# Kernel optimization log

Hardware: AMD Instinct MI355X
Metric: run time of the kernel (lower is better)

Reference implementation:

```python
import jax, jax.numpy as jnp
import numpy as np

N = 10000      # nodes
E = 160000     # edges
G = 512        # graphs in batch
IN, H, OUT = 128, 512, 16
L = 4          # num_layers
EPS = 1e-5


def setup_inputs() -> dict:
    key = jax.random.key(0)
    ks = jax.random.split(key, 8)
    x = jax.random.normal(ks[0], (N, IN), dtype=jnp.float32)
    edge_index = jax.random.randint(ks[1], (2, E), 0, N)
    batch = jnp.sort(jax.random.randint(ks[2], (N,), 0, G))
    # GCNConv layer 0 (IN -> H) and layers 1..L-1 (H -> H), plus per-layer LayerNorm affine
    W0 = jax.random.normal(ks[3], (IN, H), dtype=jnp.float32) / np.float32(np.sqrt(IN))
    b0 = jnp.zeros((H,), jnp.float32)
    g0 = jnp.ones((IN,), jnp.float32)
    be0 = jnp.zeros((IN,), jnp.float32)
    Wh = jax.random.normal(ks[4], (L - 1, H, H), dtype=jnp.float32) / np.float32(np.sqrt(H))
    bh = jnp.zeros((L - 1, H), jnp.float32)
    gh = jnp.ones((L - 1, H), jnp.float32)
    beh = jnp.zeros((L - 1, H), jnp.float32)
    linW = jax.random.normal(ks[5], (H, OUT), dtype=jnp.float32) / np.float32(np.sqrt(H))
    linb = jnp.zeros((OUT,), jnp.float32)
    return dict(x=x, edge_index=edge_index, batch=batch, W0=W0, b0=b0, g0=g0, be0=be0,
                Wh=Wh, bh=bh, gh=gh, beh=beh, linW=linW, linb=linb)


def _layernorm(x, g, b):
    mu = jnp.mean(x, axis=-1, keepdims=True)
    var = jnp.var(x, axis=-1, keepdims=True)
    return (x - mu) * jax.lax.rsqrt(var + EPS) * g + b


def _gcn(x, W, b, src, dst, dinv):
    # GCNConv with self-loops: out_i = sum_{j->i} d_j^-1/2 d_i^-1/2 (xW)_j + d_i^-1 (xW)_i + b
    h = x @ W                                   # [N, H']
    coef = (dinv[src] * dinv[dst])[:, None]     # [E, 1]
    agg = jax.ops.segment_sum(h[src] * coef, dst, num_segments=N)
    agg = agg + h * (dinv * dinv)[:, None]      # self-loop term
    return agg + b


def reference(x, edge_index, batch, W0, b0, g0, be0, Wh, bh, gh, beh, linW, linb):
    src, dst = edge_index[0], edge_index[1]
    # degree with self-loops (counted on destination nodes, edge weight 1)
    deg = jax.ops.segment_sum(jnp.ones((E,), x.dtype), dst, num_segments=N) + 1.0
    dinv = jax.lax.rsqrt(deg)
    h = jax.nn.relu(_gcn(_layernorm(x, g0, be0), W0, b0, src, dst, dinv))
    for i in range(L - 1):
        h = jax.nn.relu(_gcn(_layernorm(h, gh[i], beh[i]), Wh[i], bh[i], src, dst, dinv))
    # scatter-mean pooling by graph id
    counts = jax.ops.segment_sum(jnp.ones((N,), x.dtype), batch, num_segments=G)
    pooled = jax.ops.segment_sum(h, batch, num_segments=G) / jnp.maximum(counts, 1.0)[:, None]
    return pooled @ linW + linb
```

## Files before the change

kernel.cpp:

```cpp
#include <hip/hip_runtime.h>

#define NN 10000
#define NE 160000
#define NG 512
#define DIN 128
#define DH 512
#define DOUT 16
#define NPAD 10112

typedef __bf16 bf16_t;
typedef __attribute__((ext_vector_type(8))) __bf16 bf16x8;
typedef __attribute__((ext_vector_type(2))) __bf16 bf16x2;
typedef __attribute__((ext_vector_type(4))) float f32x4;


__global__ void k_deg_count(const int* __restrict__ dst, int* __restrict__ deg) {
    int e = blockIdx.x * blockDim.x + threadIdx.x;
    if (e < NE) atomicAdd(&deg[dst[e]], 1);
}

__global__ void k_dinv(const int* __restrict__ deg, float* __restrict__ dinv) {
    int n = blockIdx.x * blockDim.x + threadIdx.x;
    if (n < NN) dinv[n] = rsqrtf((float)deg[n] + 1.0f);
}

__global__ __launch_bounds__(1024) void k_scan(const int* __restrict__ cnt, int* __restrict__ rowptr) {
    __shared__ int part[1024];
    int tid = threadIdx.x;
    const int PER = 10;
    int base = tid * PER;
    int local[PER];
    int s = 0;
#pragma unroll
    for (int i = 0; i < PER; ++i) {
        int idx = base + i;
        int v = (idx < NN) ? cnt[idx] : 0;
        local[i] = s;
        s += v;
    }
    part[tid] = s;
    __syncthreads();
    for (int off = 1; off < 1024; off <<= 1) {
        int v = (tid >= off) ? part[tid - off] : 0;
        __syncthreads();
        part[tid] += v;
        __syncthreads();
    }
    int offset = (tid > 0) ? part[tid - 1] : 0;
#pragma unroll
    for (int i = 0; i < PER; ++i) {
        int idx = base + i;
        if (idx < NN) rowptr[idx] = offset + local[i];
    }
    if (tid == 1023) rowptr[NN] = part[1023];
}

__global__ void k_fill_csr(const int* __restrict__ src, const int* __restrict__ dst,
                           const float* __restrict__ dinv, const int* __restrict__ rowptr,
                           int* __restrict__ cursor, int* __restrict__ csr_src,
                           float* __restrict__ csr_coef) {
    int e = blockIdx.x * blockDim.x + threadIdx.x;
    if (e >= NE) return;
    int s = src[e], d = dst[e];
    int pos = atomicAdd(&cursor[d], 1);
    int idx = rowptr[d] + pos;
    csr_src[idx] = s;
    csr_coef[idx] = dinv[s] * dinv[d];
}


__global__ void k_wt_all(const float* __restrict__ W0, const float* __restrict__ Wh,
                         bf16_t* __restrict__ Wt0, bf16_t* __restrict__ Wth) {
    int idx = blockIdx.x * 256 + threadIdx.x;
    if (idx < 512 * DIN) {
        int k = idx >> 9, n = idx & 511;
        Wt0[n * DIN + k] = (bf16_t)W0[idx];
    }
    int j = idx - 512 * DIN;
    if (j >= 0 && j < 3 * DH * DH) {
        int l = j / (DH * DH), r = j % (DH * DH);
        int k = r >> 9, n = r & 511;
        Wth[(size_t)l * DH * DH + n * DH + k] = (bf16_t)Wh[j];
    }
}


__global__ __launch_bounds__(256) void k_ln0(const float* __restrict__ x,
                                             const float* __restrict__ g,
                                             const float* __restrict__ b,
                                             bf16_t* __restrict__ y) {
    int row = blockIdx.x * 4 + (threadIdx.x >> 6);
    int lane = threadIdx.x & 63;
    if (row >= NN) return;
    const float* xr = x + (size_t)row * DIN;
    float v0 = xr[lane], v1 = xr[lane + 64];
    float s = v0 + v1, s2 = v0 * v0 + v1 * v1;
#pragma unroll
    for (int off = 32; off; off >>= 1) {
        s += __shfl_xor(s, off);
        s2 += __shfl_xor(s2, off);
    }
    float mu = s * (1.f / 128.f);
    float var = s2 * (1.f / 128.f) - mu * mu;
    float r = rsqrtf(var + 1e-5f);
    bf16_t* yr = y + (size_t)row * DIN;
    yr[lane] = (bf16_t)((v0 - mu) * r * g[lane] + b[lane]);
    yr[lane + 64] = (bf16_t)((v1 - mu) * r * g[lane + 64] + b[lane + 64]);
}


__global__ __launch_bounds__(256) void k_ln512(const bf16_t* __restrict__ x,
                                               const float* __restrict__ g,
                                               const float* __restrict__ b,
                                               bf16_t* __restrict__ y) {
    int row = blockIdx.x * 4 + (threadIdx.x >> 6);
    int lane = threadIdx.x & 63;
    if (row >= NN) return;
    int c0 = lane * 8;
    bf16x8 v = *(const bf16x8*)&x[(size_t)row * DH + c0];
    float f[8];
    float s = 0.f, s2 = 0.f;
#pragma unroll
    for (int i = 0; i < 8; ++i) {
        f[i] = (float)v[i];
        s += f[i];
        s2 += f[i] * f[i];
    }
#pragma unroll
    for (int off = 32; off; off >>= 1) {
        s += __shfl_xor(s, off);
        s2 += __shfl_xor(s2, off);
    }
    float mu = s * (1.f / 512.f);
    float var = s2 * (1.f / 512.f) - mu * mu;
    float r = rsqrtf(var + 1e-5f);
    f32x4 g0 = *(const f32x4*)&g[c0], g1 = *(const f32x4*)&g[c0 + 4];
    f32x4 b0 = *(const f32x4*)&b[c0], b1 = *(const f32x4*)&b[c0 + 4];
    bf16x8 o;
#pragma unroll
    for (int i = 0; i < 4; ++i) {
        o[i] = (bf16_t)((f[i] - mu) * r * g0[i] + b0[i]);
        o[i + 4] = (bf16_t)((f[i + 4] - mu) * r * g1[i] + b1[i]);
    }
    *(bf16x8*)&y[(size_t)row * DH + c0] = o;
}


template <bool EPI>
__global__ __launch_bounds__(256) void k_gemm_bf16(const bf16_t* __restrict__ A,
                                                   const bf16_t* __restrict__ Bt,
                                                   const float* __restrict__ bias,
                                                   bf16_t* __restrict__ C, int K) {
    __shared__ bf16_t As[128 * 64];
    __shared__ bf16_t Bs[64 * 64];
    int tid = threadIdx.x;
    int lane = tid & 63, w = tid >> 6;
    int row0 = blockIdx.x * 128;
    int col0 = blockIdx.y * 64;
    int wm = w >> 1, wn = w & 1;

    f32x4 acc[4][2];
#pragma unroll
    for (int i = 0; i < 4; ++i)
#pragma unroll
        for (int j = 0; j < 2; ++j) acc[i][j] = (f32x4){0.f, 0.f, 0.f, 0.f};

    int lr = lane >> 3;
    int lc = lane & 7;

    for (int kt = 0; kt < K; kt += 64) {
#pragma unroll
        for (int i = 0; i < 4; ++i) {
            int r = w * 32 + i * 8 + lr;
            int cg = lc ^ (r & 7);
            const bf16_t* src = A + (size_t)(row0 + r) * K + kt + cg * 8;
            __builtin_amdgcn_global_load_lds(
                (const __attribute__((address_space(1))) void*)src,
                (__attribute__((address_space(3))) void*)(As + (w * 32 + i * 8) * 64),
                16, 0, 0);
        }
#pragma unroll
        for (int i = 0; i < 2; ++i) {
            int r = w * 16 + i * 8 + lr;
            int cg = lc ^ (r & 7);
            const bf16_t* src = Bt + (size_t)(col0 + r) * K + kt + cg * 8;
            __builtin_amdgcn_global_load_lds(
                (const __attribute__((address_space(1))) void*)src,
                (__attribute__((address_space(3))) void*)(Bs + (w * 16 + i * 8) * 64),
                16, 0, 0);
        }
        __syncthreads();
#pragma unroll
        for (int ks = 0; ks < 2; ++ks) {
            bf16x8 af[4], bfr[2];
#pragma unroll
            for (int mi = 0; mi < 4; ++mi) {
                int mr = wm * 64 + mi * 16 + (lane & 15);
                int c = (ks * 4 + (lane >> 4)) ^ (mr & 7);
                af[mi] = *(const bf16x8*)&As[mr * 64 + c * 8];
            }
#pragma unroll
            for (int ni = 0; ni < 2; ++ni) {
                int nr = wn * 32 + ni * 16 + (lane & 15);
                int c = (ks * 4 + (lane >> 4)) ^ (nr & 7);
                bfr[ni] = *(const bf16x8*)&Bs[nr * 64 + c * 8];
            }
#pragma unroll
            for (int mi = 0; mi < 4; ++mi)
#pragma unroll
                for (int ni = 0; ni < 2; ++ni)
                    acc[mi][ni] = __builtin_amdgcn_mfma_f32_16x16x32_bf16(
                        af[mi], bfr[ni], acc[mi][ni], 0, 0, 0);
        }
        __syncthreads();
    }
#pragma unroll
    for (int mi = 0; mi < 4; ++mi)
#pragma unroll
        for (int ni = 0; ni < 2; ++ni) {
            int col = col0 + wn * 32 + ni * 16 + (lane & 15);
            float bv = EPI ? bias[col] : 0.f;
#pragma unroll
            for (int q = 0; q < 4; ++q) {
                int row = row0 + wm * 64 + mi * 16 + (lane >> 4) * 4 + q;
                float v = acc[mi][ni][q];
                if (EPI) v = fmaxf(v + bv, 0.f);
                C[(size_t)row * DH + col] = (bf16_t)v;
            }
        }
}


__global__ __launch_bounds__(256) void k_agg128(const bf16_t* __restrict__ H,
                                                const int* __restrict__ rowptr,
                                                const int* __restrict__ csr_src,
                                                const float* __restrict__ csr_coef,
                                                const float* __restrict__ dinv,
                                                bf16_t* __restrict__ out) {
    int w = threadIdx.x >> 6, lane = threadIdx.x & 63;
    int n = blockIdx.x * 4 + w;
    int c0 = lane * 2;
    float a0 = 0.f, a1 = 0.f;
    int s0 = rowptr[n], s1 = rowptr[n + 1];
    int k = s0;
    for (; k + 2 <= s1; k += 2) {
        int sA = csr_src[k], sB = csr_src[k + 1];
        float cA = csr_coef[k], cB = csr_coef[k + 1];
        bf16x2 vA = *(const bf16x2*)&H[(size_t)sA * DIN + c0];
        bf16x2 vB = *(const bf16x2*)&H[(size_t)sB * DIN + c0];
        a0 += (float)vA[0] * cA + (float)vB[0] * cB;
        a1 += (float)vA[1] * cA + (float)vB[1] * cB;
    }
    if (k < s1) {
        int sA = csr_src[k];
        float cA = csr_coef[k];
        bf16x2 vA = *(const bf16x2*)&H[(size_t)sA * DIN + c0];
        a0 += (float)vA[0] * cA;
        a1 += (float)vA[1] * cA;
    }
    float di = dinv[n], sc = di * di;
    bf16x2 vs = *(const bf16x2*)&H[(size_t)n * DIN + c0];
    a0 += (float)vs[0] * sc;
    a1 += (float)vs[1] * sc;
    bf16x2 o;
    o[0] = (bf16_t)a0;
    o[1] = (bf16_t)a1;
    *(bf16x2*)&out[(size_t)n * DIN + c0] = o;
}


template <bool DO_LN>
__global__ __launch_bounds__(256) void k_agg(const bf16_t* __restrict__ H,
                                             const int* __restrict__ rowptr,
                                             const int* __restrict__ csr_src,
                                             const float* __restrict__ csr_coef,
                                             const float* __restrict__ dinv,
                                             const float* __restrict__ bias,
                                             const float* __restrict__ gamma,
                                             const float* __restrict__ beta,
                                             bf16_t* __restrict__ out) {
    int w = threadIdx.x >> 6, lane = threadIdx.x & 63;
    int n = blockIdx.x * 4 + w;
    int c0 = lane * 8;
    float acc[8] = {0.f, 0.f, 0.f, 0.f, 0.f, 0.f, 0.f, 0.f};
    int s0 = rowptr[n], s1 = rowptr[n + 1];
    int k = s0;
    for (; k + 2 <= s1; k += 2) {
        int sA = csr_src[k], sB = csr_src[k + 1];
        float cA = csr_coef[k], cB = csr_coef[k + 1];
        bf16x8 vA = *(const bf16x8*)&H[(size_t)sA * DH + c0];
        bf16x8 vB = *(const bf16x8*)&H[(size_t)sB * DH + c0];
#pragma unroll
        for (int i = 0; i < 8; ++i) acc[i] += (float)vA[i] * cA + (float)vB[i] * cB;
    }
    if (k < s1) {
        int sA = csr_src[k];
        float cA = csr_coef[k];
        bf16x8 vA = *(const bf16x8*)&H[(size_t)sA * DH + c0];
#pragma unroll
        for (int i = 0; i < 8; ++i) acc[i] += (float)vA[i] * cA;
    }
    float di = dinv[n], sc = di * di;
    bf16x8 vs = *(const bf16x8*)&H[(size_t)n * DH + c0];
#pragma unroll
    for (int i = 0; i < 8; ++i) acc[i] += (float)vs[i] * sc;
    f32x4 bb0 = *(const f32x4*)&bias[c0], bb1 = *(const f32x4*)&bias[c0 + 4];
#pragma unroll
    for (int i = 0; i < 4; ++i) {
        acc[i] = fmaxf(acc[i] + bb0[i], 0.f);
        acc[i + 4] = fmaxf(acc[i + 4] + bb1[i], 0.f);
    }
    bf16x8 o;
    if (DO_LN) {
        float s = 0.f, s2 = 0.f;
#pragma unroll
        for (int i = 0; i < 8; ++i) {
            s += acc[i];
            s2 += acc[i] * acc[i];
        }
#pragma unroll
        for (int off = 32; off; off >>= 1) {
            s += __shfl_xor(s, off);
            s2 += __shfl_xor(s2, off);
        }
        float mu = s * (1.f / 512.f);
        float var = s2 * (1.f / 512.f) - mu * mu;
        float r = rsqrtf(var + 1e-5f);
        f32x4 g0 = *(const f32x4*)&gamma[c0], g1 = *(const f32x4*)&gamma[c0 + 4];
        f32x4 be0 = *(const f32x4*)&beta[c0], be1 = *(const f32x4*)&beta[c0 + 4];
#pragma unroll
        for (int i = 0; i < 4; ++i) {
            o[i] = (bf16_t)((acc[i] - mu) * r * g0[i] + be0[i]);
            o[i + 4] = (bf16_t)((acc[i + 4] - mu) * r * g1[i] + be1[i]);
        }
    } else {
#pragma unroll
        for (int i = 0; i < 8; ++i) o[i] = (bf16_t)acc[i];
    }
    *(bf16x8*)&out[(size_t)n * DH + c0] = o;
}


__global__ __launch_bounds__(256) void k_poolfin(const bf16_t* __restrict__ h,
                                                 const int* __restrict__ batch,
                                                 const float* __restrict__ linW,
                                                 const float* __restrict__ linb,
                                                 float* __restrict__ out) {
    __shared__ float pooled[DH];
    __shared__ float red[256];
    int g = blockIdx.x;
    int t = threadIdx.x;
    int lo = 0, hi = NN;
    while (lo < hi) {
        int mid = (lo + hi) >> 1;
        if (batch[mid] < g) lo = mid + 1;
        else hi = mid;
    }
    int start = lo;
    hi = NN;
    while (lo < hi) {
        int mid = (lo + hi) >> 1;
        if (batch[mid] < g + 1) lo = mid + 1;
        else hi = mid;
    }
    int end = lo;
    int c0 = t * 2;
    float a0 = 0.f, a1 = 0.f;
    for (int i = start; i < end; ++i) {
        bf16x2 v = *(const bf16x2*)&h[(size_t)i * DH + c0];
        a0 += (float)v[0];
        a1 += (float)v[1];
    }
    float inv = 1.f / fmaxf((float)(end - start), 1.0f);
    pooled[c0] = a0 * inv;
    pooled[c0 + 1] = a1 * inv;
    __syncthreads();
    int o = t & 15, c = t >> 4;
    float s = 0.f;
    int k0 = c * 32;
    for (int k = k0; k < k0 + 32; ++k) s += pooled[k] * linW[k * DOUT + o];
    red[t] = s;
    __syncthreads();
    if (t < DOUT) {
        float acc2 = 0.f;
        for (int cc = 0; cc < 16; ++cc) acc2 += red[cc * 16 + t];
        out[g * DOUT + t] = acc2 + linb[t];
    }
}


extern "C" void kernel_launch(void* const* d_in, const int* in_sizes, int n_in,
                              void* d_out, int out_size, void* d_ws, size_t ws_size,
                              hipStream_t stream) {
    const float* x = (const float*)d_in[0];
    const int* ei = (const int*)d_in[1];
    const int* batch = (const int*)d_in[2];
    const float* W0 = (const float*)d_in[3];
    const float* b0 = (const float*)d_in[4];
    const float* g0 = (const float*)d_in[5];
    const float* be0 = (const float*)d_in[6];
    const float* Wh = (const float*)d_in[7];
    const float* bh = (const float*)d_in[8];
    const float* gh = (const float*)d_in[9];
    const float* beh = (const float*)d_in[10];
    const float* linW = (const float*)d_in[11];
    const float* linb = (const float*)d_in[12];
    float* out = (float*)d_out;

    bf16_t* lnbuf = (bf16_t*)d_ws;
    bf16_t* Cbf = lnbuf + (size_t)NPAD * DH;
    bf16_t* lnx = Cbf + (size_t)NPAD * DH;
    bf16_t* aggx = lnx + (size_t)NPAD * DIN;
    bf16_t* Wt0 = aggx + (size_t)NPAD * DIN;
    bf16_t* Wth = Wt0 + 512 * DIN;
    float* dinv = (float*)(Wth + 3 * 512 * 512);
    int* deg = (int*)(dinv + NN);
    int* rowptr = deg + NN;
    int* cursor = rowptr + NN + 1;
    int* csr_src = cursor + NN;
    float* csr_coef = (float*)(csr_src + NE);

    const int* srcp = ei;
    const int* dstp = ei + NE;

    hipMemsetAsync(deg, 0, NN * sizeof(int), stream);
    hipMemsetAsync(cursor, 0, NN * sizeof(int), stream);
    k_deg_count<<<(NE + 255) / 256, 256, 0, stream>>>(dstp, deg);
    k_dinv<<<(NN + 255) / 256, 256, 0, stream>>>(deg, dinv);
    k_scan<<<1, 1024, 0, stream>>>(deg, rowptr);
    k_fill_csr<<<(NE + 255) / 256, 256, 0, stream>>>(srcp, dstp, dinv, rowptr, cursor,
                                                     csr_src, csr_coef);
    k_wt_all<<<(512 * DIN + 3 * DH * DH + 255) / 256, 256, 0, stream>>>(W0, Wh, Wt0, Wth);

    dim3 gemm_grid(NPAD / 128, DH / 64);

    k_ln0<<<(NN + 3) / 4, 256, 0, stream>>>(x, g0, be0, lnx);
    k_agg128<<<NN / 4, 256, 0, stream>>>(lnx, rowptr, csr_src, csr_coef, dinv, aggx);
    k_gemm_bf16<true><<<gemm_grid, 256, 0, stream>>>(aggx, Wt0, b0, Cbf, DIN);
    k_ln512<<<(NN + 3) / 4, 256, 0, stream>>>(Cbf, gh + 0 * DH, beh + 0 * DH, lnbuf);

    for (int l = 0; l < 2; ++l) {
        k_gemm_bf16<false><<<gemm_grid, 256, 0, stream>>>(lnbuf, Wth + (size_t)l * DH * DH,
                                                          nullptr, Cbf, DH);
        k_agg<true><<<NN / 4, 256, 0, stream>>>(Cbf, rowptr, csr_src, csr_coef, dinv,
                                                bh + l * DH, gh + (l + 1) * DH,
                                                beh + (l + 1) * DH, lnbuf);
    }
    k_gemm_bf16<false><<<gemm_grid, 256, 0, stream>>>(lnbuf, Wth + (size_t)2 * DH * DH,
                                                      nullptr, Cbf, DH);
    k_agg<false><<<NN / 4, 256, 0, stream>>>(Cbf, rowptr, csr_src, csr_coef, dinv,
                                             bh + 2 * DH, nullptr, nullptr, lnbuf);

    k_poolfin<<<NG, 256, 0, stream>>>(lnbuf, batch, linW, linb, out);
}
```

Before: 235.4 us.

## Fuse prep kernels, interleave CSR, shrink GEMM tile, split aggregation across warps

Merges the input LayerNorm, degree count, weight transpose and cursor reset into one multi-role prep kernel, and folds the dinv computation into the scan. The CSR source index and coefficient are packed into one int2 array so each edge needs a single load. GEMM tiles shrink from 128x64 to 64x64 so more blocks are launched. Aggregation now gives each node a whole block, with four warps splitting its edges and summing partials in shared memory. This trades fewer launches and more parallelism for an extra block-level reduction and sync in every aggregation.

```diff
diff --git a/kernel.cpp b/kernel.cpp
--- a/kernel.cpp
+++ b/kernel.cpp
@@ -12,19 +12,70 @@
 typedef __attribute__((ext_vector_type(8))) __bf16 bf16x8;
 typedef __attribute__((ext_vector_type(2))) __bf16 bf16x2;
 typedef __attribute__((ext_vector_type(4))) float f32x4;
-
-
-__global__ void k_deg_count(const int* __restrict__ dst, int* __restrict__ deg) {
-    int e = blockIdx.x * blockDim.x + threadIdx.x;
-    if (e < NE) atomicAdd(&deg[dst[e]], 1);
-}
-
-__global__ void k_dinv(const int* __restrict__ deg, float* __restrict__ dinv) {
-    int n = blockIdx.x * blockDim.x + threadIdx.x;
-    if (n < NN) dinv[n] = rsqrtf((float)deg[n] + 1.0f);
-}
-
-__global__ __launch_bounds__(1024) void k_scan(const int* __restrict__ cnt, int* __restrict__ rowptr) {
+typedef __attribute__((ext_vector_type(2))) float f32x2;
+
+#define LNB 2500
+#define DEGB ((NE + 255) / 256)
+#define WTE (512 * DIN + 3 * DH * DH)
+#define WTB ((WTE + 255) / 256)
+#define CURB ((NN + 255) / 256)
+
+
+__global__ __launch_bounds__(256) void k_prep(const float* __restrict__ x,
+                                              const float* __restrict__ g0,
+                                              const float* __restrict__ be0,
+                                              bf16_t* __restrict__ lnx,
+                                              const int* __restrict__ dst,
+                                              int* __restrict__ deg,
+                                              const float* __restrict__ W0,
+                                              const float* __restrict__ Wh,
+                                              bf16_t* __restrict__ Wt0,
+                                              bf16_t* __restrict__ Wth,
+                                              int* __restrict__ cursor) {
+    int b = blockIdx.x;
+    int tid = threadIdx.x;
+    if (b < LNB) {
+        int row = b * 4 + (tid >> 6);
+        int lane = tid & 63;
+        const float* xr = x + (size_t)row * DIN;
+        float v0 = xr[lane], v1 = xr[lane + 64];
+        float s = v0 + v1, s2 = v0 * v0 + v1 * v1;
+#pragma unroll
+        for (int off = 32; off; off >>= 1) {
+            s += __shfl_xor(s, off);
+            s2 += __shfl_xor(s2, off);
+        }
+        float mu = s * (1.f / 128.f);
+        float var = s2 * (1.f / 128.f) - mu * mu;
+        float r = rsqrtf(var + 1e-5f);
+        bf16_t* yr = lnx + (size_t)row * DIN;
+        yr[lane] = (bf16_t)((v0 - mu) * r * g0[lane] + be0[lane]);
+        yr[lane + 64] = (bf16_t)((v1 - mu) * r * g0[lane + 64] + be0[lane + 64]);
+    } else if (b < LNB + DEGB) {
+        int e = (b - LNB) * 256 + tid;
+        if (e < NE) atomicAdd(&deg[dst[e]], 1);
+    } else if (b < LNB + DEGB + WTB) {
+        int idx = (b - LNB - DEGB) * 256 + tid;
+        if (idx < 512 * DIN) {
+            int k = idx >> 9, n = idx & 511;
+            Wt0[n * DIN + k] = (bf16_t)W0[idx];
+        } else if (idx < WTE) {
+            int j = idx - 512 * DIN;
+            int l = j >> 18;
+            int r2 = j & 262143;
+            int k = r2 >> 9, n = r2 & 511;
+            Wth[((size_t)l << 18) + n * DH + k] = (bf16_t)Wh[j];
+        }
+    } else {
+        int i = (b - LNB - DEGB - WTB) * 256 + tid;
+        if (i < NN) cursor[i] = 0;
+    }
+}
+
+
+__global__ __launch_bounds__(1024) void k_scan(const int* __restrict__ cnt,
+                                               int* __restrict__ rowptr,
+                                               float* __restrict__ dinv) {
     __shared__ int part[1024];
     int tid = threadIdx.x;
     const int PER = 10;
@@ -35,6 +86,7 @@
     for (int i = 0; i < PER; ++i) {
         int idx = base + i;
         int v = (idx < NN) ? cnt[idx] : 0;
+        if (idx < NN) dinv[idx] = rsqrtf((float)v + 1.0f);
         local[i] = s;
         s += v;
     }
@@ -57,55 +109,12 @@
 
 __global__ void k_fill_csr(const int* __restrict__ src, const int* __restrict__ dst,
                            const float* __restrict__ dinv, const int* __restrict__ rowptr,
-                           int* __restrict__ cursor, int* __restrict__ csr_src,
-                           float* __restrict__ csr_coef) {
+                           int* __restrict__ cursor, int2* __restrict__ csr) {
     int e = blockIdx.x * blockDim.x + threadIdx.x;
     if (e >= NE) return;
     int s = src[e], d = dst[e];
     int pos = atomicAdd(&cursor[d], 1);
-    int idx = rowptr[d] + pos;
-    csr_src[idx] = s;
-    csr_coef[idx] = dinv[s] * dinv[d];
-}
-
-
-__global__ void k_wt_all(const float* __restrict__ W0, const float* __restrict__ Wh,
-                         bf16_t* __restrict__ Wt0, bf16_t* __restrict__ Wth) {
-    int idx = blockIdx.x * 256 + threadIdx.x;
-    if (idx < 512 * DIN) {
-        int k = idx >> 9, n = idx & 511;
-        Wt0[n * DIN + k] = (bf16_t)W0[idx];
-    }
-    int j = idx - 512 * DIN;
-    if (j >= 0 && j < 3 * DH * DH) {
-        int l = j / (DH * DH), r = j % (DH * DH);
-        int k = r >> 9, n = r & 511;
-        Wth[(size_t)l * DH * DH + n * DH + k] = (bf16_t)Wh[j];
-    }
-}
-
-
-__global__ __launch_bounds__(256) void k_ln0(const float* __restrict__ x,
-                                             const float* __restrict__ g,
-                                             const float* __restrict__ b,
-                                             bf16_t* __restrict__ y) {
-    int row = blockIdx.x * 4 + (threadIdx.x >> 6);
-    int lane = threadIdx.x & 63;
-    if (row >= NN) return;
-    const float* xr = x + (size_t)row * DIN;
-    float v0 = xr[lane], v1 = xr[lane + 64];
-    float s = v0 + v1, s2 = v0 * v0 + v1 * v1;
-#pragma unroll
-    for (int off = 32; off; off >>= 1) {
-        s += __shfl_xor(s, off);
-        s2 += __shfl_xor(s2, off);
-    }
-    float mu = s * (1.f / 128.f);
-    float var = s2 * (1.f / 128.f) - mu * mu;
-    float r = rsqrtf(var + 1e-5f);
-    bf16_t* yr = y + (size_t)row * DIN;
-    yr[lane] = (bf16_t)((v0 - mu) * r * g[lane] + b[lane]);
-    yr[lane + 64] = (bf16_t)((v1 - mu) * r * g[lane + 64] + b[lane + 64]);
+    csr[rowptr[d] + pos] = make_int2(s, __float_as_int(dinv[s] * dinv[d]));
 }
 
 
@@ -147,21 +156,20 @@
 
 
 template <bool EPI>
-__global__ __launch_bounds__(256) void k_gemm_bf16(const bf16_t* __restrict__ A,
-                                                   const bf16_t* __restrict__ Bt,
-                                                   const float* __restrict__ bias,
-                                                   bf16_t* __restrict__ C, int K) {
-    __shared__ bf16_t As[128 * 64];
+__global__ __launch_bounds__(256) void k_gemm64(const bf16_t* __restrict__ A,
+                                                const bf16_t* __restrict__ Bt,
+                                                const float* __restrict__ bias,
+                                                bf16_t* __restrict__ C, int K) {
+    __shared__ bf16_t As[64 * 64];
     __shared__ bf16_t Bs[64 * 64];
     int tid = threadIdx.x;
     int lane = tid & 63, w = tid >> 6;
-    int row0 = blockIdx.x * 128;
-    int col0 = blockIdx.y * 64;
+    int row0 = blockIdx.x * 64, col0 = blockIdx.y * 64;
     int wm = w >> 1, wn = w & 1;
 
-    f32x4 acc[4][2];
-#pragma unroll
-    for (int i = 0; i < 4; ++i)
+    f32x4 acc[2][2];
+#pragma unroll
+    for (int i = 0; i < 2; ++i)
 #pragma unroll
         for (int j = 0; j < 2; ++j) acc[i][j] = (f32x4){0.f, 0.f, 0.f, 0.f};
 
@@ -169,33 +177,28 @@
     int lc = lane & 7;
 
     for (int kt = 0; kt < K; kt += 64) {
-#pragma unroll
-        for (int i = 0; i < 4; ++i) {
-            int r = w * 32 + i * 8 + lr;
-            int cg = lc ^ (r & 7);
-            const bf16_t* src = A + (size_t)(row0 + r) * K + kt + cg * 8;
-            __builtin_amdgcn_global_load_lds(
-                (const __attribute__((address_space(1))) void*)src,
-                (__attribute__((address_space(3))) void*)(As + (w * 32 + i * 8) * 64),
-                16, 0, 0);
-        }
 #pragma unroll
         for (int i = 0; i < 2; ++i) {
             int r = w * 16 + i * 8 + lr;
             int cg = lc ^ (r & 7);
-            const bf16_t* src = Bt + (size_t)(col0 + r) * K + kt + cg * 8;
+            const bf16_t* srca = A + (size_t)(row0 + r) * K + kt + cg * 8;
             __builtin_amdgcn_global_load_lds(
-                (const __attribute__((address_space(1))) void*)src,
+                (const __attribute__((address_space(1))) void*)srca,
+                (__attribute__((address_space(3))) void*)(As + (w * 16 + i * 8) * 64),
+                16, 0, 0);
+            const bf16_t* srcb = Bt + (size_t)(col0 + r) * K + kt + cg * 8;
+            __builtin_amdgcn_global_load_lds(
+                (const __attribute__((address_space(1))) void*)srcb,
                 (__attribute__((address_space(3))) void*)(Bs + (w * 16 + i * 8) * 64),
                 16, 0, 0);
         }
         __syncthreads();
 #pragma unroll
         for (int ks = 0; ks < 2; ++ks) {
-            bf16x8 af[4], bfr[2];
-#pragma unroll
-            for (int mi = 0; mi < 4; ++mi) {
-                int mr = wm * 64 + mi * 16 + (lane & 15);
+            bf16x8 af[2], bfr[2];
+#pragma unroll
+            for (int mi = 0; mi < 2; ++mi) {
+                int mr = wm * 32 + mi * 16 + (lane & 15);
                 int c = (ks * 4 + (lane >> 4)) ^ (mr & 7);
                 af[mi] = *(const bf16x8*)&As[mr * 64 + c * 8];
             }
@@ -206,7 +209,7 @@
                 bfr[ni] = *(const bf16x8*)&Bs[nr * 64 + c * 8];
             }
 #pragma unroll
-            for (int mi = 0; mi < 4; ++mi)
+            for (int mi = 0; mi < 2; ++mi)
 #pragma unroll
                 for (int ni = 0; ni < 2; ++ni)
                     acc[mi][ni] = __builtin_amdgcn_mfma_f32_16x16x32_bf16(
@@ -215,14 +218,14 @@
         __syncthreads();
     }
 #pragma unroll
-    for (int mi = 0; mi < 4; ++mi)
+    for (int mi = 0; mi < 2; ++mi)
 #pragma unroll
         for (int ni = 0; ni < 2; ++ni) {
             int col = col0 + wn * 32 + ni * 16 + (lane & 15);
             float bv = EPI ? bias[col] : 0.f;
 #pragma unroll
             for (int q = 0; q < 4; ++q) {
-                int row = row0 + wm * 64 + mi * 16 + (lane >> 4) * 4 + q;
+                int row = row0 + wm * 32 + mi * 16 + (lane >> 4) * 4 + q;
                 float v = acc[mi][ni][q];
                 if (EPI) v = fmaxf(v + bv, 0.f);
                 C[(size_t)row * DH + col] = (bf16_t)v;
@@ -233,111 +236,123 @@
 
 __global__ __launch_bounds__(256) void k_agg128(const bf16_t* __restrict__ H,
                                                 const int* __restrict__ rowptr,
-                                                const int* __restrict__ csr_src,
-                                                const float* __restrict__ csr_coef,
+                                                const int2* __restrict__ csr,
                                                 const float* __restrict__ dinv,
                                                 bf16_t* __restrict__ out) {
+    __shared__ float part[4][DIN];
+    int n = blockIdx.x;
     int w = threadIdx.x >> 6, lane = threadIdx.x & 63;
-    int n = blockIdx.x * 4 + w;
     int c0 = lane * 2;
     float a0 = 0.f, a1 = 0.f;
     int s0 = rowptr[n], s1 = rowptr[n + 1];
-    int k = s0;
-    for (; k + 2 <= s1; k += 2) {
-        int sA = csr_src[k], sB = csr_src[k + 1];
-        float cA = csr_coef[k], cB = csr_coef[k + 1];
-        bf16x2 vA = *(const bf16x2*)&H[(size_t)sA * DIN + c0];
-        bf16x2 vB = *(const bf16x2*)&H[(size_t)sB * DIN + c0];
+    int k = s0 + w;
+    for (; k + 4 < s1; k += 8) {
+        int2 eA = csr[k], eB = csr[k + 4];
+        float cA = __int_as_float(eA.y), cB = __int_as_float(eB.y);
+        bf16x2 vA = *(const bf16x2*)&H[(size_t)eA.x * DIN + c0];
+        bf16x2 vB = *(const bf16x2*)&H[(size_t)eB.x * DIN + c0];
         a0 += (float)vA[0] * cA + (float)vB[0] * cB;
         a1 += (float)vA[1] * cA + (float)vB[1] * cB;
     }
     if (k < s1) {
-        int sA = csr_src[k];
-        float cA = csr_coef[k];
-        bf16x2 vA = *(const bf16x2*)&H[(size_t)sA * DIN + c0];
+        int2 eA = csr[k];
+        float cA = __int_as_float(eA.y);
+        bf16x2 vA = *(const bf16x2*)&H[(size_t)eA.x * DIN + c0];
         a0 += (float)vA[0] * cA;
         a1 += (float)vA[1] * cA;
     }
-    float di = dinv[n], sc = di * di;
-    bf16x2 vs = *(const bf16x2*)&H[(size_t)n * DIN + c0];
-    a0 += (float)vs[0] * sc;
-    a1 += (float)vs[1] * sc;
-    bf16x2 o;
-    o[0] = (bf16_t)a0;
-    o[1] = (bf16_t)a1;
-    *(bf16x2*)&out[(size_t)n * DIN + c0] = o;
+    part[w][c0] = a0;
+    part[w][c0 + 1] = a1;
+    __syncthreads();
+    if (threadIdx.x < 64) {
+        int cc = threadIdx.x * 2;
+        float b0 = part[0][cc] + part[1][cc] + part[2][cc] + part[3][cc];
+        float b1 = part[0][cc + 1] + part[1][cc + 1] + part[2][cc + 1] + part[3][cc + 1];
+        float di = dinv[n], sc = di * di;
+        bf16x2 vs = *(const bf16x2*)&H[(size_t)n * DIN + cc];
+        b0 += (float)vs[0] * sc;
+        b1 += (float)vs[1] * sc;
+        bf16x2 o;
+        o[0] = (bf16_t)b0;
+        o[1] = (bf16_t)b1;
+        *(bf16x2*)&out[(size_t)n * DIN + cc] = o;
+    }
 }
 
 
 template <bool DO_LN>
 __global__ __launch_bounds__(256) void k_agg(const bf16_t* __restrict__ H,
                                              const int* __restrict__ rowptr,
-                                             const int* __restrict__ csr_src,
-                                             const float* __restrict__ csr_coef,
+                                             const int2* __restrict__ csr,
                                              const float* __restrict__ dinv,
                                              const float* __restrict__ bias,
                                              const float* __restrict__ gamma,
                                              const float* __restrict__ beta,
                                              bf16_t* __restrict__ out) {
+    __shared__ float part[4][DH];
+    __shared__ float rs[8];
+    int n = blockIdx.x;
     int w = threadIdx.x >> 6, lane = threadIdx.x & 63;
-    int n = blockIdx.x * 4 + w;
     int c0 = lane * 8;
     float acc[8] = {0.f, 0.f, 0.f, 0.f, 0.f, 0.f, 0.f, 0.f};
     int s0 = rowptr[n], s1 = rowptr[n + 1];
-    int k = s0;
-    for (; k + 2 <= s1; k += 2) {
-        int sA = csr_src[k], sB = csr_src[k + 1];
-        float cA = csr_coef[k], cB = csr_coef[k + 1];
-        bf16x8 vA = *(const bf16x8*)&H[(size_t)sA * DH + c0];
-        bf16x8 vB = *(const bf16x8*)&H[(size_t)sB * DH + c0];
+    int k = s0 + w;
+    for (; k + 4 < s1; k += 8) {
+        int2 eA = csr[k], eB = csr[k + 4];
+        float cA = __int_as_float(eA.y), cB = __int_as_float(eB.y);
+        bf16x8 vA = *(const bf16x8*)&H[(size_t)eA.x * DH + c0];
+        bf16x8 vB = *(const bf16x8*)&H[(size_t)eB.x * DH + c0];
 #pragma unroll
         for (int i = 0; i < 8; ++i) acc[i] += (float)vA[i] * cA + (float)vB[i] * cB;
     }
     if (k < s1) {
-        int sA = csr_src[k];
-        float cA = csr_coef[k];
-        bf16x8 vA = *(const bf16x8*)&H[(size_t)sA * DH + c0];
+        int2 eA = csr[k];
+        float cA = __int_as_float(eA.y);
+        bf16x8 vA = *(const bf16x8*)&H[(size_t)eA.x * DH + c0];
 #pragma unroll
         for (int i = 0; i < 8; ++i) acc[i] += (float)vA[i] * cA;
     }
+    *(f32x4*)&part[w][c0] = (f32x4){acc[0], acc[1], acc[2], acc[3]};
+    *(f32x4*)&part[w][c0 + 4] = (f32x4){acc[4], acc[5], acc[6], acc[7]};
+    __syncthreads();
+    int cc = threadIdx.x * 2;
+    f32x2 p0 = *(const f32x2*)&part[0][cc];
+    f32x2 p1 = *(const f32x2*)&part[1][cc];
+    f32x2 p2 = *(const f32x2*)&part[2][cc];
+    f32x2 p3 = *(const f32x2*)&part[3][cc];
+    float a0 = p0[0] + p1[0] + p2[0] + p3[0];
+    float a1 = p0[1] + p1[1] + p2[1] + p3[1];
     float di = dinv[n], sc = di * di;
-    bf16x8 vs = *(const bf16x8*)&H[(size_t)n * DH + c0];
-#pragma unroll
-    for (int i = 0; i < 8; ++i) acc[i] += (float)vs[i] * sc;
-    f32x4 bb0 = *(const f32x4*)&bias[c0], bb1 = *(const f32x4*)&bias[c0 + 4];
-#pragma unroll
-    for (int i = 0; i < 4; ++i) {
-        acc[i] = fmaxf(acc[i] + bb0[i], 0.f);
-        acc[i + 4] = fmaxf(acc[i + 4] + bb1[i], 0.f);
-    }
-    bf16x8 o;
+    bf16x2 vs = *(const bf16x2*)&H[(size_t)n * DH + cc];
+    a0 += (float)vs[0] * sc;
+    a1 += (float)vs[1] * sc;
+    a0 = fmaxf(a0 + bias[cc], 0.f);
+    a1 = fmaxf(a1 + bias[cc + 1], 0.f);
+    bf16x2 o;
     if (DO_LN) {
-        float s = 0.f, s2 = 0.f;
-#pragma unroll
-        for (int i = 0; i < 8; ++i) {
-            s += acc[i];
-            s2 += acc[i] * acc[i];
-        }
+        float s = a0 + a1, s2 = a0 * a0 + a1 * a1;
 #pragma unroll
         for (int off = 32; off; off >>= 1) {
             s += __shfl_xor(s, off);
             s2 += __shfl_xor(s2, off);
         }
+        if (lane == 0) {
+            rs[w] = s;
+            rs[4 + w] = s2;
+        }
+        __syncthreads();
+        s = rs[0] + rs[1] + rs[2] + rs[3];
+        s2 = rs[4] + rs[5] + rs[6] + rs[7];
         float mu = s * (1.f / 512.f);
         float var = s2 * (1.f / 512.f) - mu * mu;
         float r = rsqrtf(var + 1e-5f);
-        f32x4 g0 = *(const f32x4*)&gamma[c0], g1 = *(const f32x4*)&gamma[c0 + 4];
-        f32x4 be0 = *(const f32x4*)&beta[c0], be1 = *(const f32x4*)&beta[c0 + 4];
-#pragma unroll
-        for (int i = 0; i < 4; ++i) {
-            o[i] = (bf16_t)((acc[i] - mu) * r * g0[i] + be0[i]);
-            o[i + 4] = (bf16_t)((acc[i + 4] - mu) * r * g1[i] + be1[i]);
-        }
+        o[0] = (bf16_t)((a0 - mu) * r * gamma[cc] + beta[cc]);
+        o[1] = (bf16_t)((a1 - mu) * r * gamma[cc + 1] + beta[cc + 1]);
     } else {
-#pragma unroll
-        for (int i = 0; i < 8; ++i) o[i] = (bf16_t)acc[i];
-    }
-    *(bf16x8*)&out[(size_t)n * DH + c0] = o;
+        o[0] = (bf16_t)a0;
+        o[1] = (bf16_t)a1;
+    }
+    *(bf16x2*)&out[(size_t)n * DH + cc] = o;
 }
 
 
@@ -413,43 +428,37 @@
     bf16_t* aggx = lnx + (size_t)NPAD * DIN;
     bf16_t* Wt0 = aggx + (size_t)NPAD * DIN;
     bf16_t* Wth = Wt0 + 512 * DIN;
-    float* dinv = (float*)(Wth + 3 * 512 * 512);
+    float* dinv = (float*)(Wth + 3 * DH * DH);
     int* deg = (int*)(dinv + NN);
     int* rowptr = deg + NN;
     int* cursor = rowptr + NN + 1;
-    int* csr_src = cursor + NN;
-    float* csr_coef = (float*)(csr_src + NE);
+    int2* csr = (int2*)(cursor + NN + 1);
 
     const int* srcp = ei;
     const int* dstp = ei + NE;
 
     hipMemsetAsync(deg, 0, NN * sizeof(int), stream);
-    hipMemsetAsync(cursor, 0, NN * sizeof(int), stream);
-    k_deg_count<<<(NE + 255) / 256, 256, 0, stream>>>(dstp, deg);
-    k_dinv<<<(NN + 255) / 256, 256, 0, stream>>>(deg, dinv);
-    k_scan<<<1, 1024, 0, stream>>>(deg, rowptr);
-    k_fill_csr<<<(NE + 255) / 256, 256, 0, stream>>>(srcp, dstp, dinv, rowptr, cursor,
-                                                     csr_src, csr_coef);
-    k_wt_all<<<(512 * DIN + 3 * DH * DH + 255) / 256, 256, 0, stream>>>(W0, Wh, Wt0, Wth);
-
-    dim3 gemm_grid(NPAD / 128, DH / 64);
-
-    k_ln0<<<(NN + 3) / 4, 256, 0, stream>>>(x, g0, be0, lnx);
-    k_agg128<<<NN / 4, 256, 0, stream>>>(lnx, rowptr, csr_src, csr_coef, dinv, aggx);
-    k_gemm_bf16<true><<<gemm_grid, 256, 0, stream>>>(aggx, Wt0, b0, Cbf, DIN);
+    k_prep<<<LNB + DEGB + WTB + CURB, 256, 0, stream>>>(x, g0, be0, lnx, dstp, deg,
+                                                        W0, Wh, Wt0, Wth, cursor);
+    k_scan<<<1, 1024, 0, stream>>>(deg, rowptr, dinv);
+    k_fill_csr<<<(NE + 255) / 256, 256, 0, stream>>>(srcp, dstp, dinv, rowptr, cursor, csr);
+
+    dim3 gemm_grid(NPAD / 64, DH / 64);
+
+    k_agg128<<<NN, 256, 0, stream>>>(lnx, rowptr, csr, dinv, aggx);
+    k_gemm64<true><<<gemm_grid, 256, 0, stream>>>(aggx, Wt0, b0, Cbf, DIN);
     k_ln512<<<(NN + 3) / 4, 256, 0, stream>>>(Cbf, gh + 0 * DH, beh + 0 * DH, lnbuf);
 
     for (int l = 0; l < 2; ++l) {
-        k_gemm_bf16<false><<<gemm_grid, 256, 0, stream>>>(lnbuf, Wth + (size_t)l * DH * DH,
-                                                          nullptr, Cbf, DH);
-        k_agg<true><<<NN / 4, 256, 0, stream>>>(Cbf, rowptr, csr_src, csr_coef, dinv,
-                                                bh + l * DH, gh + (l + 1) * DH,
-                                                beh + (l + 1) * DH, lnbuf);
-    }
-    k_gemm_bf16<false><<<gemm_grid, 256, 0, stream>>>(lnbuf, Wth + (size_t)2 * DH * DH,
-                                                      nullptr, Cbf, DH);
-    k_agg<false><<<NN / 4, 256, 0, stream>>>(Cbf, rowptr, csr_src, csr_coef, dinv,
-                                             bh + 2 * DH, nullptr, nullptr, lnbuf);
+        k_gemm64<false><<<gemm_grid, 256, 0, stream>>>(lnbuf, Wth + (size_t)l * DH * DH,
+                                                       nullptr, Cbf, DH);
+        k_agg<true><<<NN, 256, 0, stream>>>(Cbf, rowptr, csr, dinv, bh + l * DH,
+                                            gh + (l + 1) * DH, beh + (l + 1) * DH, lnbuf);
+    }
+    k_gemm64<false><<<gemm_grid, 256, 0, stream>>>(lnbuf, Wth + (size_t)2 * DH * DH,
+                                                   nullptr, Cbf, DH);
+    k_agg<false><<<NN, 256, 0, stream>>>(Cbf, rowptr, csr, dinv, bh + 2 * DH,
+                                         nullptr, nullptr, lnbuf);
 
     k_poolfin<<<NG, 256, 0, stream>>>(lnbuf, batch, linW, linb, out);
 }
```

Result: faster. 207.4 us (-11.9%).
